# Performance work log

Hardware: AMD Instinct MI355X
Metric: run time of the kernel (lower is better)

## Reference

```python
import jax, jax.numpy as jnp
import numpy as np

DIM = 192
HEADS = 6
PE_TABLE_SIZE = 2601  # 51x51 relative-position grid, rows of length pos_dim+3=5


def setup_inputs() -> dict:
    key = jax.random.key(0)
    ks = jax.random.split(key, 16)
    b, n, m, c = 2, 8192, 48, DIM
    feat = jax.random.normal(ks[0], (b, n, c), dtype=jnp.float32)
    member_idx = jax.random.randint(ks[1], (b, n, m), 0, n)
    cluster_mask = (jax.random.uniform(ks[2], (b, n, m)) > 0.1).astype(jnp.float32)
    pe_idx = jax.random.randint(ks[3], (b, n, m), 0, PE_TABLE_SIZE)
    s = 1.0 / np.sqrt(c)
    Wq = jax.random.normal(ks[4], (c, c), dtype=jnp.float32) * s
    bq = jnp.zeros((c,), jnp.float32)
    Wkv = jax.random.normal(ks[5], (2 * c, c), dtype=jnp.float32) * s
    bkv = jnp.zeros((2 * c,), jnp.float32)
    Wpe = jax.random.normal(ks[6], (HEADS, 5), dtype=jnp.float32) * 0.4
    bpe = jnp.zeros((HEADS,), jnp.float32)
    blank_k = jax.random.normal(ks[7], (c,), dtype=jnp.float32)
    blank_v = jax.random.normal(ks[8], (c,), dtype=jnp.float32)
    Wproj = jax.random.normal(ks[9], (c, c), dtype=jnp.float32) * s
    bproj = jnp.zeros((c,), jnp.float32)
    pre_table = jax.random.normal(ks[10], (PE_TABLE_SIZE, 5), dtype=jnp.float32)
    return {"feat": feat, "member_idx": member_idx, "cluster_mask": cluster_mask,
            "pe_idx": pe_idx, "global_attn": 0,
            "Wq": Wq, "bq": bq, "Wkv": Wkv, "bkv": bkv, "Wpe": Wpe, "bpe": bpe,
            "blank_k": blank_k, "blank_v": blank_v, "Wproj": Wproj, "bproj": bproj,
            "pre_table": pre_table}


def reference(feat, member_idx, cluster_mask, pe_idx, global_attn,
              Wq, bq, Wkv, bkv, Wpe, bpe, blank_k, blank_v, Wproj, bproj, pre_table):
    b, n, c = feat.shape
    h = Wpe.shape[0]
    c_ = c // h
    scale = c_ ** (-0.5)

    q = (feat @ Wq.T + bq) * scale                      # [b,n,c]
    kv = (feat @ Wkv.T + bkv).reshape(b, n, h, 2, c_)   # split like torch view(b,n,h,2,c_)
    k = kv[:, :, :, 0, :]                               # [b,n,h,c_]
    v = kv[:, :, :, 1, :]                               # [b,n,h,c_]
    q = q.reshape(b, n, h, c_)

    # positional-embedding lookup table: [T,5] -> [T,h]
    pe_table = pre_table @ Wpe.T + bpe
    pos = pe_table[pe_idx]                              # [b,n,m,h]

    if not global_attn:
        m = member_idx.shape[-1]
        idx = member_idx.reshape(b, n * m, 1)
        # gather neighbor keys/values: CLUSTENQK / CLUSTENAV semantics
        kg = jnp.take_along_axis(k.reshape(b, n, h * c_), idx, axis=1).reshape(b, n, m, h, c_)
        attn = jnp.einsum('bnhc,bnmhc->bhnm', q, kg)    # [b,h,n,m]
        attn = attn + pos.transpose(0, 3, 1, 2)
        attn = attn + (1.0 - cluster_mask)[:, None] * (-100.0)
    else:
        attn = jnp.einsum('bnhc,bshc->bhns', q, k)
        attn = attn + pos.transpose(0, 3, 1, 2)

    # blank token logit, clamped
    blank = jnp.clip(jnp.einsum('bnhc,hc->bhn', q, blank_k.reshape(h, c_)), -5.0, 5.0)[..., None]
    attn_all = jax.nn.softmax(jnp.concatenate([attn, blank], axis=-1), axis=-1)
    attn_nb = attn_all[..., :-1]                        # [b,h,n,m]
    blank_a = attn_all[..., -1:]                        # [b,h,n,1]

    if not global_attn:
        vg = jnp.take_along_axis(v.reshape(b, n, h * c_), idx, axis=1).reshape(b, n, m, h, c_)
        out = jnp.einsum('bhnm,bnmhc->bnhc', attn_nb, vg)
    else:
        out = jnp.einsum('bhns,bshc->bnhc', attn_nb, v)

    out = out + blank_a.transpose(0, 2, 1, 3) * blank_v.reshape(1, 1, h, c_)
    out = out.reshape(b, n, c)
    return out @ Wproj.T + bproj
```

## Files before the change

kernel.cpp:

```cpp
#include <hip/hip_runtime.h>
#include <hip/hip_fp16.h>

#define DIMC 192
#define HEADS 6
#define NSEQ 8192
#define NB 2
#define NMEM 48
#define PE_N 2601
#define NTOT (NB * NSEQ)

typedef _Float16 f16;
typedef __attribute__((ext_vector_type(4))) _Float16 f16x4;
typedef __attribute__((ext_vector_type(8))) _Float16 f16x8;
typedef __attribute__((ext_vector_type(4))) float f32x4;
typedef __attribute__((ext_vector_type(4))) int i32x4;

__global__ void pe_kernel(const float* __restrict__ pre_table,
                          const float* __restrict__ Wpe,
                          const float* __restrict__ bpe,
                          float* __restrict__ pe_out) {
    int i = blockIdx.x * blockDim.x + threadIdx.x;
    if (i >= PE_N) return;
    float p0 = pre_table[i * 5 + 0], p1 = pre_table[i * 5 + 1], p2 = pre_table[i * 5 + 2];
    float p3 = pre_table[i * 5 + 3], p4 = pre_table[i * 5 + 4];
#pragma unroll
    for (int h = 0; h < HEADS; ++h) {
        float s = bpe[h] + p0 * Wpe[h * 5 + 0] + p1 * Wpe[h * 5 + 1] + p2 * Wpe[h * 5 + 2]
                + p3 * Wpe[h * 5 + 3] + p4 * Wpe[h * 5 + 4];
        pe_out[i * HEADS + h] = s;
    }
}

#define FEAT4 (NTOT * DIMC / 4)
#define WQ4   (DIMC * DIMC / 4)
#define WKV4  (2 * DIMC * DIMC / 4)
#define BL4   (DIMC / 4)
__global__ __launch_bounds__(256) void cvt_kernel(
    const float* __restrict__ feat, const float* __restrict__ Wq,
    const float* __restrict__ Wkv, const float* __restrict__ Wproj,
    const float* __restrict__ blank_k, const float* __restrict__ blank_v,
    f16* __restrict__ featH, f16* __restrict__ WqH, f16* __restrict__ WkvH,
    f16* __restrict__ WprojH, f16* __restrict__ bkH, f16* __restrict__ bvH) {
    const int total = FEAT4 + WQ4 + WKV4 + WQ4 + BL4 + BL4;
    for (int i = blockIdx.x * 256 + threadIdx.x; i < total; i += gridDim.x * 256) {
        const float* src; f16* dst; int j = i;
        if (j < FEAT4)             { src = feat;    dst = featH; }
        else if ((j -= FEAT4) < WQ4)  { src = Wq;      dst = WqH; }
        else if ((j -= WQ4) < WKV4)   { src = Wkv;     dst = WkvH; }
        else if ((j -= WKV4) < WQ4)   { src = Wproj;   dst = WprojH; }
        else if ((j -= WQ4) < BL4)    { src = blank_k; dst = bkH; }
        else { j -= BL4;              src = blank_v;   dst = bvH; }
        float4 f = *reinterpret_cast<const float4*>(src + (size_t)j * 4);
        f16x4 h = {(f16)f.x, (f16)f.y, (f16)f.z, (f16)f.w};
        *reinterpret_cast<f16x4*>(dst + (size_t)j * 4) = h;
    }
}

__global__ __launch_bounds__(256) void gemm16_kernel(
    const f16* __restrict__ A, const f16* __restrict__ Wa, const f16* __restrict__ Wb,
    const float* __restrict__ b0, const float* __restrict__ bkv,
    f16* __restrict__ oq, f16* __restrict__ ok, f16* __restrict__ ov,
    float* __restrict__ ofp, const int mode) {
    __shared__ f16 As[64 * DIMC];
    __shared__ f16 Bs[64 * DIMC];
    const int tid = threadIdx.x, w = tid >> 6, l = tid & 63;
    const size_t rowbase = (size_t)blockIdx.x * 64;
    const int colbase = blockIdx.y * 64;
    const f16* Wsel = (mode == 0 && colbase >= DIMC) ? (Wb + (size_t)(colbase - DIMC) * DIMC)
                                                     : (Wa + (size_t)colbase * DIMC);
    const char* Abase = (const char*)(A + rowbase * DIMC);
    const char* Wbase = (const char*)Wsel;
#pragma unroll
    for (int i = 0; i < 6; ++i) {
        const int L = (w * 6 + i) * 64 + l;
        const int row = L / 24, cp = L % 24;
        const int coff = ((cp ^ (row & 7)) << 4);
        __builtin_amdgcn_global_load_lds(
            (const __attribute__((address_space(1))) unsigned int*)(Abase + row * 384 + coff),
            (__attribute__((address_space(3))) unsigned int*)(As + (size_t)(w * 6 + i) * 512),
            16, 0, 0);
        __builtin_amdgcn_global_load_lds(
            (const __attribute__((address_space(1))) unsigned int*)(Wbase + row * 384 + coff),
            (__attribute__((address_space(3))) unsigned int*)(Bs + (size_t)(w * 6 + i) * 512),
            16, 0, 0);
    }
    __syncthreads();
    const int lm = l & 15, lg = l >> 4, sw = l & 7;
    const int wr = w & 1, wc = w >> 1;
    f32x4 acc[2][2];
    acc[0][0] = acc[0][1] = acc[1][0] = acc[1][1] = (f32x4){0.f, 0.f, 0.f, 0.f};
    const char* AsB = (const char*)As;
    const char* BsB = (const char*)Bs;
    const int ar0 = (wr * 32 + lm) * 384, ar1 = (wr * 32 + 16 + lm) * 384;
    const int br0 = (wc * 32 + lm) * 384, br1 = (wc * 32 + 16 + lm) * 384;
#pragma unroll
    for (int ks = 0; ks < 6; ++ks) {
        const int ch = ((ks * 4 + lg) ^ sw) << 4;
        f16x8 a0 = *reinterpret_cast<const f16x8*>(AsB + ar0 + ch);
        f16x8 a1 = *reinterpret_cast<const f16x8*>(AsB + ar1 + ch);
        f16x8 q0 = *reinterpret_cast<const f16x8*>(BsB + br0 + ch);
        f16x8 q1 = *reinterpret_cast<const f16x8*>(BsB + br1 + ch);
        acc[0][0] = __builtin_amdgcn_mfma_f32_16x16x32_f16(a0, q0, acc[0][0], 0, 0, 0);
        acc[0][1] = __builtin_amdgcn_mfma_f32_16x16x32_f16(a0, q1, acc[0][1], 0, 0, 0);
        acc[1][0] = __builtin_amdgcn_mfma_f32_16x16x32_f16(a1, q0, acc[1][0], 0, 0, 0);
        acc[1][1] = __builtin_amdgcn_mfma_f32_16x16x32_f16(a1, q1, acc[1][1], 0, 0, 0);
    }
#pragma unroll
    for (int fm = 0; fm < 2; ++fm)
#pragma unroll
        for (int fn = 0; fn < 2; ++fn) {
            const int col = colbase + wc * 32 + fn * 16 + lm;
            const size_t r0 = rowbase + wr * 32 + fm * 16 + lg * 4;
            if (mode == 1) {
                const float bias = b0[col];
#pragma unroll
                for (int r = 0; r < 4; ++r)
                    ofp[(r0 + r) * DIMC + col] = acc[fm][fn][r] + bias;
            } else if (col < DIMC) {
                const float bias = b0[col];
#pragma unroll
                for (int r = 0; r < 4; ++r)
                    oq[(r0 + r) * DIMC + col] =
                        (f16)((acc[fm][fn][r] + bias) * 0.17677669529663687f);
            } else {
                const int t0 = col - DIMC;
                const float bias = bkv[t0];
                const int hh = t0 >> 6, rr = t0 & 63;
                f16* dst = (rr < 32) ? (ok + hh * 32 + rr) : (ov + hh * 32 + (rr - 32));
#pragma unroll
                for (int r = 0; r < 4; ++r)
                    dst[(r0 + r) * DIMC] = (f16)(acc[fm][fn][r] + bias);
            }
        }
}

__global__ __launch_bounds__(256) void attn_kernel(
    const f16* __restrict__ qH, const f16* __restrict__ kH, const f16* __restrict__ vH,
    const f16* __restrict__ bkH, const f16* __restrict__ bvH,
    const int* __restrict__ member_idx, const float* __restrict__ cmask,
    const int* __restrict__ pe_idx, const float* __restrict__ peT,
    f16* __restrict__ outA) {
    __shared__ float p_lds[4][HEADS][64];
    __shared__ int m_lds[4][64];
    const int wave = threadIdx.x >> 6, lane = threadIdx.x & 63;
    const int qi = blockIdx.x * 4 + wave;
    const int bbase = qi & ~(NSEQ - 1);
    if (lane < NMEM)
        m_lds[wave][lane] = bbase + member_idx[(size_t)qi * NMEM + lane];
    __syncthreads();
    const int s = lane & 1, ms = lane >> 1;
    const f16* qbase = qH + (size_t)qi * DIMC + s * 96;
#pragma unroll
    for (int pass = 0; pass < 2; ++pass) {
        const int m = pass * 32 + ms;
        const bool act = (m <= NMEM);
        const f16* kp;
        if (act && m < NMEM) kp = kH + (size_t)m_lds[wave][m] * DIMC + s * 96;
        else                 kp = bkH + s * 96;
        float a0 = 0.f, a1 = 0.f, a2 = 0.f;
#pragma unroll
        for (int j = 0; j < 12; ++j) {
            f16x8 qv = *reinterpret_cast<const f16x8*>(qbase + j * 8);
            f16x8 kd = *reinterpret_cast<const f16x8*>(kp + j * 8);
            float d = (float)qv[0] * (float)kd[0] + (float)qv[1] * (float)kd[1]
                    + (float)qv[2] * (float)kd[2] + (float)qv[3] * (float)kd[3]
                    + (float)qv[4] * (float)kd[4] + (float)qv[5] * (float)kd[5]
                    + (float)qv[6] * (float)kd[6] + (float)qv[7] * (float)kd[7];
            if (j < 4)      a0 += d;
            else if (j < 8) a1 += d;
            else            a2 += d;
        }
        if (act) {
            p_lds[wave][3 * s + 0][m] = a0;
            p_lds[wave][3 * s + 1][m] = a1;
            p_lds[wave][3 * s + 2][m] = a2;
        }
    }
    __syncthreads();
    {
        const int m = lane;
        float lo[HEADS];
#pragma unroll
        for (int h = 0; h < HEADS; ++h)
            lo[h] = (m <= NMEM) ? p_lds[wave][h][m] : -1e30f;
        if (m < NMEM) {
            const int pei = pe_idx[(size_t)qi * NMEM + m];
            const float msk = (1.0f - cmask[(size_t)qi * NMEM + m]) * -100.0f;
#pragma unroll
            for (int h = 0; h < HEADS; ++h) lo[h] += peT[pei * HEADS + h] + msk;
        } else if (m == NMEM) {
#pragma unroll
            for (int h = 0; h < HEADS; ++h) lo[h] = fminf(fmaxf(lo[h], -5.f), 5.f);
        }
#pragma unroll
        for (int h = 0; h < HEADS; ++h) {
            float mx = lo[h];
#pragma unroll
            for (int st = 32; st; st >>= 1) mx = fmaxf(mx, __shfl_xor(mx, st));
            const float e = __expf(lo[h] - mx);
            float sm = e;
#pragma unroll
            for (int st = 32; st; st >>= 1) sm += __shfl_xor(sm, st);
            p_lds[wave][h][m] = e / sm;
        }
    }
    __syncthreads();
    const int h0 = lane >> 5;
    float o0 = 0.f, o1 = 0.f, o2 = 0.f;
#pragma unroll 4
    for (int mm = 0; mm < NMEM; mm += 4) {
        const i32x4 rows = *reinterpret_cast<const i32x4*>(&m_lds[wave][mm]);
        const f32x4 w0 = *reinterpret_cast<const f32x4*>(&p_lds[wave][h0][mm]);
        const f32x4 w1 = *reinterpret_cast<const f32x4*>(&p_lds[wave][h0 + 2][mm]);
        const f32x4 w2 = *reinterpret_cast<const f32x4*>(&p_lds[wave][h0 + 4][mm]);
#pragma unroll
        for (int t = 0; t < 4; ++t) {
            const f16* vp = vH + (size_t)rows[t] * DIMC;
            o0 += w0[t] * (float)vp[lane];
            o1 += w1[t] * (float)vp[64 + lane];
            o2 += w2[t] * (float)vp[128 + lane];
        }
    }
    o0 += p_lds[wave][h0][NMEM]     * (float)bvH[lane];
    o1 += p_lds[wave][h0 + 2][NMEM] * (float)bvH[64 + lane];
    o2 += p_lds[wave][h0 + 4][NMEM] * (float)bvH[128 + lane];
    f16* orow = outA + (size_t)qi * DIMC;
    orow[lane] = (f16)o0; orow[64 + lane] = (f16)o1; orow[128 + lane] = (f16)o2;
}

extern "C" void kernel_launch(void* const* d_in, const int* in_sizes, int n_in,
                              void* d_out, int out_size, void* d_ws, size_t ws_size,
                              hipStream_t stream) {
    const float* feat      = (const float*)d_in[0];
    const int*   member_i  = (const int*)d_in[1];
    const float* cmask     = (const float*)d_in[2];
    const int*   pe_idx    = (const int*)d_in[3];
    const float* Wq        = (const float*)d_in[5];
    const float* bq        = (const float*)d_in[6];
    const float* Wkv       = (const float*)d_in[7];
    const float* bkv       = (const float*)d_in[8];
    const float* Wpe       = (const float*)d_in[9];
    const float* bpe       = (const float*)d_in[10];
    const float* blank_k   = (const float*)d_in[11];
    const float* blank_v   = (const float*)d_in[12];
    const float* Wproj     = (const float*)d_in[13];
    const float* bproj     = (const float*)d_in[14];
    const float* pre_table = (const float*)d_in[15];
    float* out = (float*)d_out;

    const size_t SZH = (size_t)NTOT * DIMC * sizeof(f16);
    char* ws = (char*)d_ws;
    f16* qH     = (f16*)(ws);
    f16* kH     = (f16*)(ws + SZH);
    f16* vH     = (f16*)(ws + 2 * SZH);
    f16* outAH  = (f16*)(ws + 3 * SZH);
    f16* featH  = (f16*)(ws + 4 * SZH);
    char* p = ws + 5 * SZH;
    f16* WqH    = (f16*)p;              p += (size_t)DIMC * DIMC * 2;
    f16* WkvH   = (f16*)p;              p += (size_t)2 * DIMC * DIMC * 2;
    f16* WprojH = (f16*)p;              p += (size_t)DIMC * DIMC * 2;
    f16* bkH    = (f16*)p;              p += 512;
    f16* bvH    = (f16*)p;              p += 512;
    float* peT  = (float*)p;            p += (size_t)PE_N * HEADS * sizeof(float);
    if ((size_t)(p - ws) > ws_size) return;

    pe_kernel<<<(PE_N + 255) / 256, 256, 0, stream>>>(pre_table, Wpe, bpe, peT);
    cvt_kernel<<<1024, 256, 0, stream>>>(feat, Wq, Wkv, Wproj, blank_k, blank_v,
                                         featH, WqH, WkvH, WprojH, bkH, bvH);
    gemm16_kernel<<<dim3(NTOT / 64, 9), 256, 0, stream>>>(
        featH, WqH, WkvH, bq, bkv, qH, kH, vH, nullptr, 0);
    attn_kernel<<<NTOT / 4, 256, 0, stream>>>(qH, kH, vH, bkH, bvH, member_i, cmask,
                                              pe_idx, peT, outAH);
    gemm16_kernel<<<dim3(NTOT / 64, 3), 256, 0, stream>>>(
        outAH, WprojH, nullptr, bproj, nullptr, nullptr, nullptr, nullptr, out, 1);
}
```

Before: 185.9 us.

## Reuse A tile across many column tiles, drop wave-local barriers, use fdot2

The GEMM kernel is templated so each block loads its A tile once and sweeps many output column tiles. Weight fragments are read straight from global/cache instead of LDS, which cuts repeated A loads across the grid and the B staging in shared memory. In the attention kernel, block-wide barriers are removed because each wave only touches its own LDS slice. The q·k dot products use packed fp16 fdot2, and the V loop unroll is increased. The trade-offs are more registers per thread and fewer blocks for the GEMMs, which could lower occupancy.

```diff
diff --git a/kernel.cpp b/kernel.cpp
--- a/kernel.cpp
+++ b/kernel.cpp
@@ -10,10 +10,21 @@
 #define NTOT (NB * NSEQ)
 
 typedef _Float16 f16;
+typedef __attribute__((ext_vector_type(2))) _Float16 f16x2;
 typedef __attribute__((ext_vector_type(4))) _Float16 f16x4;
 typedef __attribute__((ext_vector_type(8))) _Float16 f16x8;
 typedef __attribute__((ext_vector_type(4))) float f32x4;
 typedef __attribute__((ext_vector_type(4))) int i32x4;
+
+static __device__ __forceinline__ float fdot2(f16x8 a, f16x8 b, int t, float acc) {
+    f16x2 ap = {a[2 * t], a[2 * t + 1]};
+    f16x2 bp = {b[2 * t], b[2 * t + 1]};
+#if __has_builtin(__builtin_amdgcn_fdot2)
+    return __builtin_amdgcn_fdot2(ap, bp, acc, false);
+#else
+    return acc + (float)ap[0] * (float)bp[0] + (float)ap[1] * (float)bp[1];
+#endif
+}
 
 __global__ void pe_kernel(const float* __restrict__ pre_table,
                           const float* __restrict__ Wpe,
@@ -56,20 +67,16 @@
     }
 }
 
+template <int CFS, int MODE>
 __global__ __launch_bounds__(256) void gemm16_kernel(
-    const f16* __restrict__ A, const f16* __restrict__ Wa, const f16* __restrict__ Wb,
+    const f16* __restrict__ A, const f16* __restrict__ W0, const f16* __restrict__ Wkv,
     const float* __restrict__ b0, const float* __restrict__ bkv,
     f16* __restrict__ oq, f16* __restrict__ ok, f16* __restrict__ ov,
-    float* __restrict__ ofp, const int mode) {
+    float* __restrict__ ofp) {
     __shared__ f16 As[64 * DIMC];
-    __shared__ f16 Bs[64 * DIMC];
     const int tid = threadIdx.x, w = tid >> 6, l = tid & 63;
     const size_t rowbase = (size_t)blockIdx.x * 64;
-    const int colbase = blockIdx.y * 64;
-    const f16* Wsel = (mode == 0 && colbase >= DIMC) ? (Wb + (size_t)(colbase - DIMC) * DIMC)
-                                                     : (Wa + (size_t)colbase * DIMC);
     const char* Abase = (const char*)(A + rowbase * DIMC);
-    const char* Wbase = (const char*)Wsel;
 #pragma unroll
     for (int i = 0; i < 6; ++i) {
         const int L = (w * 6 + i) * 64 + l;
@@ -79,59 +86,69 @@
             (const __attribute__((address_space(1))) unsigned int*)(Abase + row * 384 + coff),
             (__attribute__((address_space(3))) unsigned int*)(As + (size_t)(w * 6 + i) * 512),
             16, 0, 0);
-        __builtin_amdgcn_global_load_lds(
-            (const __attribute__((address_space(1))) unsigned int*)(Wbase + row * 384 + coff),
-            (__attribute__((address_space(3))) unsigned int*)(Bs + (size_t)(w * 6 + i) * 512),
-            16, 0, 0);
     }
     __syncthreads();
-    const int lm = l & 15, lg = l >> 4, sw = l & 7;
+    const int lm = l & 15, lg = l >> 4;
     const int wr = w & 1, wc = w >> 1;
-    f32x4 acc[2][2];
-    acc[0][0] = acc[0][1] = acc[1][0] = acc[1][1] = (f32x4){0.f, 0.f, 0.f, 0.f};
+    const int r0 = wr * 32 + lm, r1 = r0 + 16;
     const char* AsB = (const char*)As;
-    const char* BsB = (const char*)Bs;
-    const int ar0 = (wr * 32 + lm) * 384, ar1 = (wr * 32 + 16 + lm) * 384;
-    const int br0 = (wc * 32 + lm) * 384, br1 = (wc * 32 + 16 + lm) * 384;
+    f16x8 af0[6], af1[6];
 #pragma unroll
     for (int ks = 0; ks < 6; ++ks) {
-        const int ch = ((ks * 4 + lg) ^ sw) << 4;
-        f16x8 a0 = *reinterpret_cast<const f16x8*>(AsB + ar0 + ch);
-        f16x8 a1 = *reinterpret_cast<const f16x8*>(AsB + ar1 + ch);
-        f16x8 q0 = *reinterpret_cast<const f16x8*>(BsB + br0 + ch);
-        f16x8 q1 = *reinterpret_cast<const f16x8*>(BsB + br1 + ch);
-        acc[0][0] = __builtin_amdgcn_mfma_f32_16x16x32_f16(a0, q0, acc[0][0], 0, 0, 0);
-        acc[0][1] = __builtin_amdgcn_mfma_f32_16x16x32_f16(a0, q1, acc[0][1], 0, 0, 0);
-        acc[1][0] = __builtin_amdgcn_mfma_f32_16x16x32_f16(a1, q0, acc[1][0], 0, 0, 0);
-        acc[1][1] = __builtin_amdgcn_mfma_f32_16x16x32_f16(a1, q1, acc[1][1], 0, 0, 0);
-    }
-#pragma unroll
-    for (int fm = 0; fm < 2; ++fm)
-#pragma unroll
-        for (int fn = 0; fn < 2; ++fn) {
-            const int col = colbase + wc * 32 + fn * 16 + lm;
-            const size_t r0 = rowbase + wr * 32 + fm * 16 + lg * 4;
-            if (mode == 1) {
+        const int ch = ((ks * 4 + lg) ^ (lm & 7)) << 4;
+        af0[ks] = *reinterpret_cast<const f16x8*>(AsB + r0 * 384 + ch);
+        af1[ks] = *reinterpret_cast<const f16x8*>(AsB + r1 * 384 + ch);
+    }
+    const int cf0 = (blockIdx.y * 2 + wc) * CFS * 16;
+    const f16* wl[CFS];
+#pragma unroll
+    for (int i = 0; i < CFS; ++i) {
+        const int col0 = cf0 + i * 16;
+        const f16* wrow = (MODE == 0 && col0 >= DIMC) ? (Wkv + (size_t)(col0 - DIMC) * DIMC)
+                                                      : (W0 + (size_t)col0 * DIMC);
+        wl[i] = wrow + (size_t)lm * DIMC + lg * 8;
+    }
+    f32x4 accA[CFS], accB[CFS];
+#pragma unroll
+    for (int i = 0; i < CFS; ++i) accA[i] = accB[i] = (f32x4){0.f, 0.f, 0.f, 0.f};
+#pragma unroll
+    for (int ks = 0; ks < 6; ++ks) {
+#pragma unroll
+        for (int i = 0; i < CFS; ++i) {
+            f16x8 bf = *reinterpret_cast<const f16x8*>(wl[i] + ks * 32);
+            accA[i] = __builtin_amdgcn_mfma_f32_16x16x32_f16(af0[ks], bf, accA[i], 0, 0, 0);
+            accB[i] = __builtin_amdgcn_mfma_f32_16x16x32_f16(af1[ks], bf, accB[i], 0, 0, 0);
+        }
+    }
+#pragma unroll
+    for (int i = 0; i < CFS; ++i) {
+        const int col = cf0 + i * 16 + lm;
+#pragma unroll
+        for (int fm = 0; fm < 2; ++fm) {
+            const f32x4 acc = fm ? accB[i] : accA[i];
+            const size_t rr0 = rowbase + wr * 32 + fm * 16 + lg * 4;
+            if (MODE == 1) {
                 const float bias = b0[col];
 #pragma unroll
                 for (int r = 0; r < 4; ++r)
-                    ofp[(r0 + r) * DIMC + col] = acc[fm][fn][r] + bias;
+                    ofp[(rr0 + r) * DIMC + col] = acc[r] + bias;
             } else if (col < DIMC) {
                 const float bias = b0[col];
 #pragma unroll
                 for (int r = 0; r < 4; ++r)
-                    oq[(r0 + r) * DIMC + col] =
-                        (f16)((acc[fm][fn][r] + bias) * 0.17677669529663687f);
+                    oq[(rr0 + r) * DIMC + col] =
+                        (f16)((acc[r] + bias) * 0.17677669529663687f);
             } else {
                 const int t0 = col - DIMC;
                 const float bias = bkv[t0];
-                const int hh = t0 >> 6, rr = t0 & 63;
-                f16* dst = (rr < 32) ? (ok + hh * 32 + rr) : (ov + hh * 32 + (rr - 32));
+                const int hh = t0 >> 6, rrm = t0 & 63;
+                f16* dst = (rrm < 32) ? (ok + hh * 32 + rrm) : (ov + hh * 32 + (rrm - 32));
 #pragma unroll
                 for (int r = 0; r < 4; ++r)
-                    dst[(r0 + r) * DIMC] = (f16)(acc[fm][fn][r] + bias);
+                    dst[(rr0 + r) * DIMC] = (f16)(acc[r] + bias);
             }
         }
+    }
 }
 
 __global__ __launch_bounds__(256) void attn_kernel(
@@ -147,7 +164,6 @@
     const int bbase = qi & ~(NSEQ - 1);
     if (lane < NMEM)
         m_lds[wave][lane] = bbase + member_idx[(size_t)qi * NMEM + lane];
-    __syncthreads();
     const int s = lane & 1, ms = lane >> 1;
     const f16* qbase = qH + (size_t)qi * DIMC + s * 96;
 #pragma unroll
@@ -162,10 +178,9 @@
         for (int j = 0; j < 12; ++j) {
             f16x8 qv = *reinterpret_cast<const f16x8*>(qbase + j * 8);
             f16x8 kd = *reinterpret_cast<const f16x8*>(kp + j * 8);
-            float d = (float)qv[0] * (float)kd[0] + (float)qv[1] * (float)kd[1]
-                    + (float)qv[2] * (float)kd[2] + (float)qv[3] * (float)kd[3]
-                    + (float)qv[4] * (float)kd[4] + (float)qv[5] * (float)kd[5]
-                    + (float)qv[6] * (float)kd[6] + (float)qv[7] * (float)kd[7];
+            float d = 0.f;
+#pragma unroll
+            for (int t = 0; t < 4; ++t) d = fdot2(qv, kd, t, d);
             if (j < 4)      a0 += d;
             else if (j < 8) a1 += d;
             else            a2 += d;
@@ -176,7 +191,6 @@
             p_lds[wave][3 * s + 2][m] = a2;
         }
     }
-    __syncthreads();
     {
         const int m = lane;
         float lo[HEADS];
@@ -204,10 +218,9 @@
             p_lds[wave][h][m] = e / sm;
         }
     }
-    __syncthreads();
     const int h0 = lane >> 5;
     float o0 = 0.f, o1 = 0.f, o2 = 0.f;
-#pragma unroll 4
+#pragma unroll 6
     for (int mm = 0; mm < NMEM; mm += 4) {
         const i32x4 rows = *reinterpret_cast<const i32x4*>(&m_lds[wave][mm]);
         const f32x4 w0 = *reinterpret_cast<const f32x4*>(&p_lds[wave][h0][mm]);
@@ -267,10 +280,10 @@
     pe_kernel<<<(PE_N + 255) / 256, 256, 0, stream>>>(pre_table, Wpe, bpe, peT);
     cvt_kernel<<<1024, 256, 0, stream>>>(feat, Wq, Wkv, Wproj, blank_k, blank_v,
                                          featH, WqH, WkvH, WprojH, bkH, bvH);
-    gemm16_kernel<<<dim3(NTOT / 64, 9), 256, 0, stream>>>(
-        featH, WqH, WkvH, bq, bkv, qH, kH, vH, nullptr, 0);
+    gemm16_kernel<9, 0><<<dim3(NTOT / 64, 2), 256, 0, stream>>>(
+        featH, WqH, WkvH, bq, bkv, qH, kH, vH, nullptr);
     attn_kernel<<<NTOT / 4, 256, 0, stream>>>(qH, kH, vH, bkH, bvH, member_i, cmask,
                                               pe_idx, peT, outAH);
-    gemm16_kernel<<<dim3(NTOT / 64, 3), 256, 0, stream>>>(
-        outAH, WprojH, nullptr, bproj, nullptr, nullptr, nullptr, nullptr, out, 1);
-}
+    gemm16_kernel<6, 1><<<dim3(NTOT / 64, 1), 256, 0, stream>>>(
+        outAH, WprojH, nullptr, bproj, nullptr, nullptr, nullptr, nullptr, out);
+}
```

Result: slower. 239.7 us (+28.9%).
